# Optimization experiments

Hardware: AMD Instinct MI355X
Metric: run time of the kernel (lower is better)

Reference implementation:

```python
import jax, jax.numpy as jnp
import numpy as np


def setup_inputs() -> dict:
    key = jax.random.key(0)
    ks = jax.random.split(key, 7)
    B, S, D, H = 8, 1024, 1024, 16
    dk = D // H
    return {
        "q": jax.random.normal(ks[0], (B, S, D), dtype=jnp.float32),
        "k": jax.random.normal(ks[1], (B, S, D), dtype=jnp.float32),
        "v": jax.random.normal(ks[2], (B, S, D), dtype=jnp.float32),
        "Wq": jax.random.normal(ks[3], (H, dk, D), dtype=jnp.float32) * 0.03,
        "Wk": jax.random.normal(ks[4], (H, dk, D), dtype=jnp.float32) * 0.03,
        "Wv": jax.random.normal(ks[5], (dk, D), dtype=jnp.float32) * 0.03,
        "Wo": jax.random.normal(ks[6], (D, dk), dtype=jnp.float32) * 0.03,
    }


def reference(q, k, v, Wq, Wk, Wv, Wo):
    # per-head projections (Linear weight layout [out, in]); shared V projection
    dk = Wq.shape[1]
    qs = jnp.einsum("bsd,hed->bhse", q, Wq)          # [B,H,S,dk]
    ks_ = jnp.einsum("btd,hed->bhte", k, Wk)         # [B,H,S,dk]
    vs = jnp.einsum("btd,ed->bte", v, Wv)            # [B,S,dk] shared across heads
    scale = jnp.sqrt(jnp.asarray(dk, dtype=qs.dtype))
    scores = jnp.einsum("bhse,bhte->bhst", qs, ks_) / scale
    attn = jax.nn.softmax(scores, axis=-1)           # [B,H,Sq,Sk]
    heads = jnp.einsum("bhst,bte->bhse", attn, vs)   # [B,H,S,dk]
    head_mean = jnp.mean(heads, axis=1)              # mean over heads -> [B,S,dk]
    outputs = jnp.einsum("bse,de->bsd", head_mean, Wo)
    attn_out = jnp.transpose(attn, (0, 2, 1, 3))     # stacked at dim=2: [B,Sq,H,Sk]
    return outputs, attn_out
```

## Files before the change

### kernel.cpp

```cpp
#include <hip/hip_runtime.h>
#include <hip/hip_bf16.h>


typedef __attribute__((ext_vector_type(4))) float f32x4;
typedef __attribute__((ext_vector_type(8))) short bf16x8;
typedef __attribute__((ext_vector_type(4))) short short4v;
typedef __attribute__((ext_vector_type(2))) unsigned int uint2v;

#define MFMA16(a, b, c) __builtin_amdgcn_mfma_f32_16x16x32_bf16((a), (b), (c), 0, 0, 0)

__device__ __forceinline__ unsigned int rne16(float f) {
  unsigned int u = __float_as_uint(f);
  return u + 0x7fffu + ((u >> 16) & 1u);
}
__device__ __forceinline__ unsigned int pack2bf(float a, float b) {
  return (rne16(a) >> 16) | (rne16(b) & 0xffff0000u);
}
__device__ __forceinline__ short f2bf(float f) {
  return (short)(rne16(f) >> 16);
}
__device__ __forceinline__ float bf2f(short s) {
  return __uint_as_float(((unsigned int)(unsigned short)s) << 16);
}

__global__ __launch_bounds__(256) void proj_qk_kernel(
    const float* __restrict__ qin, const float* __restrict__ kin,
    const float* __restrict__ Wq, const float* __restrict__ Wk,
    __hip_bfloat16* __restrict__ qs, __hip_bfloat16* __restrict__ ks)
{
  const int K = 1024, N = 1024;
  __shared__ short a_lds[128][40];
  __shared__ short b_lds[128][40];
  const int tid  = threadIdx.x;
  const int lane = tid & 63, wid = tid >> 6;
  const int g = lane >> 4, r = lane & 15;
  const bool isK = blockIdx.y >= 8;
  const float* A = isK ? kin : qin;
  const float* W = isK ? Wk : Wq;
  __hip_bfloat16* C = isK ? ks : qs;
  const float scale = isK ? 1.0f : 0.125f;
  const int m0 = blockIdx.x * 128;
  const int n0 = (blockIdx.y & 7) * 128;
  const int wm = (wid >> 1) * 64, wn = (wid & 1) * 64;
  const int lrow = tid >> 3, lcol = (tid & 7) * 4;

  f32x4 acc[4][4];
#pragma unroll
  for (int i = 0; i < 4; ++i)
#pragma unroll
    for (int j = 0; j < 4; ++j) acc[i][j] = (f32x4){0.f, 0.f, 0.f, 0.f};

  for (int k0 = 0; k0 < K; k0 += 32) {
    float4 av[4], wv[4];
#pragma unroll
    for (int p = 0; p < 4; ++p) {
      av[p] = *(const float4*)&A[(m0 + lrow + p * 32) * K + k0 + lcol];
      wv[p] = *(const float4*)&W[(n0 + lrow + p * 32) * K + k0 + lcol];
    }
    __syncthreads();
#pragma unroll
    for (int p = 0; p < 4; ++p) {
      uint2v ua = {pack2bf(av[p].x, av[p].y), pack2bf(av[p].z, av[p].w)};
      uint2v uw = {pack2bf(wv[p].x, wv[p].y), pack2bf(wv[p].z, wv[p].w)};
      *(uint2v*)&a_lds[lrow + p * 32][lcol] = ua;
      *(uint2v*)&b_lds[lrow + p * 32][lcol] = uw;
    }
    __syncthreads();
    bf16x8 af[4], bf[4];
#pragma unroll
    for (int t = 0; t < 4; ++t) {
      af[t] = *(bf16x8*)&a_lds[wm + t * 16 + r][g * 8];
      bf[t] = *(bf16x8*)&b_lds[wn + t * 16 + r][g * 8];
    }
#pragma unroll
    for (int mt = 0; mt < 4; ++mt)
#pragma unroll
      for (int nt = 0; nt < 4; ++nt)
        acc[mt][nt] = MFMA16(af[mt], bf[nt], acc[mt][nt]);
  }

#pragma unroll
  for (int mt = 0; mt < 4; ++mt)
#pragma unroll
    for (int nt = 0; nt < 4; ++nt) {
      const int n = n0 + wn + nt * 16 + r;
#pragma unroll
      for (int j = 0; j < 4; ++j) {
        const int m = m0 + wm + mt * 16 + 4 * g + j;
        C[m * N + n] = __float2bfloat16(acc[mt][nt][j] * scale);
      }
    }
}

__global__ __launch_bounds__(256) void proj_v_kernel(
    const float* __restrict__ vin, const float* __restrict__ Wv,
    __hip_bfloat16* __restrict__ vsT)
{
  const int K = 1024;
  __shared__ short a_lds[128][40];
  __shared__ short b_lds[64][40];
  const int tid  = threadIdx.x;
  const int lane = tid & 63, wid = tid >> 6;
  const int g = lane >> 4, r = lane & 15;
  const int m0 = blockIdx.x * 128;
  const int wm = wid * 32;
  const int lrow = tid >> 3, lcol = (tid & 7) * 4;

  f32x4 acc[2][4];
#pragma unroll
  for (int i = 0; i < 2; ++i)
#pragma unroll
    for (int j = 0; j < 4; ++j) acc[i][j] = (f32x4){0.f, 0.f, 0.f, 0.f};

  for (int k0 = 0; k0 < K; k0 += 32) {
    float4 av[4], wv2[2];
#pragma unroll
    for (int p = 0; p < 4; ++p)
      av[p] = *(const float4*)&vin[(m0 + lrow + p * 32) * K + k0 + lcol];
#pragma unroll
    for (int p = 0; p < 2; ++p)
      wv2[p] = *(const float4*)&Wv[(lrow + p * 32) * K + k0 + lcol];
    __syncthreads();
#pragma unroll
    for (int p = 0; p < 4; ++p) {
      uint2v ua = {pack2bf(av[p].x, av[p].y), pack2bf(av[p].z, av[p].w)};
      *(uint2v*)&a_lds[lrow + p * 32][lcol] = ua;
    }
#pragma unroll
    for (int p = 0; p < 2; ++p) {
      uint2v uw = {pack2bf(wv2[p].x, wv2[p].y), pack2bf(wv2[p].z, wv2[p].w)};
      *(uint2v*)&b_lds[lrow + p * 32][lcol] = uw;
    }
    __syncthreads();
    bf16x8 af[2], bf[4];
#pragma unroll
    for (int t = 0; t < 2; ++t) af[t] = *(bf16x8*)&a_lds[wm + t * 16 + r][g * 8];
#pragma unroll
    for (int t = 0; t < 4; ++t) bf[t] = *(bf16x8*)&b_lds[t * 16 + r][g * 8];
#pragma unroll
    for (int mt = 0; mt < 2; ++mt)
#pragma unroll
      for (int nt = 0; nt < 4; ++nt)
        acc[mt][nt] = MFMA16(af[mt], bf[nt], acc[mt][nt]);
  }

#pragma unroll
  for (int mt = 0; mt < 2; ++mt)
#pragma unroll
    for (int nt = 0; nt < 4; ++nt) {
      const int e = nt * 16 + r;
#pragma unroll
      for (int j = 0; j < 4; ++j) {
        const int m = m0 + wm + mt * 16 + 4 * g + j;
        const int b = m >> 10, t = m & 1023;
        vsT[b * 65536 + e * 1024 + t] = __float2bfloat16(acc[mt][nt][j]);
      }
    }
}

__global__ __launch_bounds__(256, 4) void attn_kernel(
    const __hip_bfloat16* __restrict__ qs_, const __hip_bfloat16* __restrict__ ks_,
    const __hip_bfloat16* __restrict__ vsT_, float* __restrict__ attn_out,
    __hip_bfloat16* __restrict__ heads_)
{
  const int S = 1024, H = 16;
  const int tid = threadIdx.x, lane = tid & 63, kc = tid >> 6;
  const int g = lane >> 4, r = lane & 15;
  const int h = blockIdx.y, b = blockIdx.z;
  const int bh = b * H + h;
  const int qrow = blockIdx.x * 16;

  __shared__ short p_big[4][16][260];
  __shared__ float l_lds[4][16];
  __shared__ float inv_lds[16];
  float (*heads_ov)[16][80] = (float (*)[16][80])p_big;

  const short* qsp = (const short*)qs_;
  const short* ksp = (const short*)ks_;
  const short* vsp = (const short*)vsT_;
  short* headsp = (short*)heads_;

  const int qidx = (b * S + qrow + r) * 1024 + h * 64;
  const bf16x8 qf0 = *(const bf16x8*)&qsp[qidx + g * 8];
  const bf16x8 qf1 = *(const bf16x8*)&qsp[qidx + 32 + g * 8];
  const int kbase = (b * S + kc * 256 + r) * 1024 + h * 64 + g * 8;

  unsigned int pk[32];
  float lsa0 = 0.f, lsa1 = 0.f, lsa2 = 0.f, lsa3 = 0.f;
#pragma unroll
  for (int i = 0; i < 4; ++i) {
    const int t0 = i * 64;
    bf16x8 kf[8];
#pragma unroll
    for (int u = 0; u < 4; ++u) {
      kf[2 * u]     = *(const bf16x8*)&ksp[kbase + (t0 + 16 * u) * 1024];
      kf[2 * u + 1] = *(const bf16x8*)&ksp[kbase + (t0 + 16 * u) * 1024 + 32];
    }
    float es[4];
#pragma unroll
    for (int u = 0; u < 4; ++u) {
      f32x4 s = (f32x4){0.f, 0.f, 0.f, 0.f};
      s = MFMA16(kf[2 * u], qf0, s);
      s = MFMA16(kf[2 * u + 1], qf1, s);
      const float e0 = __expf(s[0]), e1 = __expf(s[1]);
      const float e2 = __expf(s[2]), e3 = __expf(s[3]);
      pk[i * 8 + 2 * u]     = pack2bf(e0, e1);
      pk[i * 8 + 2 * u + 1] = pack2bf(e2, e3);
      es[u] = (e0 + e1) + (e2 + e3);
    }
    lsa0 += es[0]; lsa1 += es[1]; lsa2 += es[2]; lsa3 += es[3];
  }
  float ls = (lsa0 + lsa1) + (lsa2 + lsa3);
  ls += __shfl_xor(ls, 16);
  ls += __shfl_xor(ls, 32);
  if (g == 0) l_lds[kc][r] = ls;
  __syncthreads();
  {
    const float lf = (l_lds[0][r] + l_lds[1][r]) + (l_lds[2][r] + l_lds[3][r]);
    if (kc == 0 && g == 0) inv_lds[r] = 1.f / lf;
  }

#pragma unroll
  for (int j = 0; j < 8; ++j) {
    uint2v w0 = {pk[4 * j + 0], pk[4 * j + 1]};
    uint2v w1 = {pk[4 * j + 2], pk[4 * j + 3]};
    *(uint2v*)&p_big[kc][r][j * 32 + 4 * g] = w0;
    *(uint2v*)&p_big[kc][r][j * 32 + 16 + 4 * g] = w1;
  }
  __syncthreads();

  f32x4 hacc[4];
#pragma unroll
  for (int i = 0; i < 4; ++i) hacc[i] = (f32x4){0.f, 0.f, 0.f, 0.f};
  const int vbase = b * 65536 + r * 1024 + g * 8 + kc * 256;

#pragma unroll
  for (int j = 0; j < 8; ++j) {
    const int tcl = j * 32;
    bf16x8 vf[4];
#pragma unroll
    for (int nt = 0; nt < 4; ++nt)
      vf[nt] = *(const bf16x8*)&vsp[vbase + nt * 16384 + tcl];
    const bf16x8 pa = *(bf16x8*)&p_big[kc][r][tcl + g * 8];
#pragma unroll
    for (int nt = 0; nt < 4; ++nt)
      hacc[nt] = MFMA16(pa, vf[nt], hacc[nt]);
  }

  {
    const int half = lane >> 5, l32 = lane & 31;
#pragma unroll
    for (int rp = 0; rp < 8; ++rp) {
      const int row = rp * 2 + half;
      const bf16x8 pe = *(const bf16x8*)&p_big[kc][row][l32 * 8];
      const float invr = inv_lds[row];
      f32x4 o0, o1;
      o0[0] = bf2f(pe[0]) * invr; o0[1] = bf2f(pe[1]) * invr;
      o0[2] = bf2f(pe[2]) * invr; o0[3] = bf2f(pe[3]) * invr;
      o1[0] = bf2f(pe[4]) * invr; o1[1] = bf2f(pe[5]) * invr;
      o1[2] = bf2f(pe[6]) * invr; o1[3] = bf2f(pe[7]) * invr;
      const int base = ((b * S + qrow + row) * H + h) * S + kc * 256 + l32 * 8;
      __builtin_nontemporal_store(o0, (f32x4*)&attn_out[base]);
      __builtin_nontemporal_store(o1, (f32x4*)&attn_out[base + 4]);
    }
  }
  __syncthreads();

#pragma unroll
  for (int nt = 0; nt < 4; ++nt)
#pragma unroll
    for (int j = 0; j < 4; ++j)
      heads_ov[kc][4 * g + j][nt * 16 + r] = hacc[nt][j];
  __syncthreads();

  {
    const int row = tid >> 4, c4 = (tid & 15) * 4;
    const float invr = inv_lds[row];
    short4v hv;
#pragma unroll
    for (int i = 0; i < 4; ++i) {
      const float s4 = (heads_ov[0][row][c4 + i] + heads_ov[1][row][c4 + i]) +
                       (heads_ov[2][row][c4 + i] + heads_ov[3][row][c4 + i]);
      hv[i] = f2bf(s4 * invr);
    }
    *(short4v*)&headsp[(bh * S + qrow + row) * 64 + c4] = hv;
  }
}

__global__ __launch_bounds__(256) void out_kernel(
    const __hip_bfloat16* __restrict__ heads_, const float* __restrict__ Wo,
    float* __restrict__ out)
{
  __shared__ float hm[16][64];
  const int tid = threadIdx.x;
  const int m0 = blockIdx.x * 16;
  const short* headsp = (const short*)heads_;

  {
    const int row = tid >> 4, e4 = (tid & 15) * 4;
    const int m = m0 + row, b = m >> 10, s = m & 1023;
    float a0 = 0.f, a1 = 0.f, a2 = 0.f, a3 = 0.f;
    for (int hh = 0; hh < 16; ++hh) {
      const short4v hv =
          *(const short4v*)&headsp[((b * 16 + hh) * 1024 + s) * 64 + e4];
      a0 += bf2f(hv[0]); a1 += bf2f(hv[1]); a2 += bf2f(hv[2]); a3 += bf2f(hv[3]);
    }
    const float sc = 1.f / 16.f;
    hm[row][e4 + 0] = a0 * sc; hm[row][e4 + 1] = a1 * sc;
    hm[row][e4 + 2] = a2 * sc; hm[row][e4 + 3] = a3 * sc;
  }
  __syncthreads();

  for (int c = 0; c < 4; ++c) {
    const int d = c * 256 + tid;
    float4 wo4[16];
#pragma unroll
    for (int i = 0; i < 16; ++i) wo4[i] = *(const float4*)&Wo[d * 64 + i * 4];
    for (int row = 0; row < 16; ++row) {
      float a = 0.f;
#pragma unroll
      for (int i = 0; i < 16; ++i) {
        const float4 h4 = *(const float4*)&hm[row][i * 4];
        a += h4.x * wo4[i].x + h4.y * wo4[i].y + h4.z * wo4[i].z + h4.w * wo4[i].w;
      }
      out[(m0 + row) * 1024 + d] = a;
    }
  }
}

extern "C" void kernel_launch(void* const* d_in, const int* in_sizes, int n_in,
                              void* d_out, int out_size, void* d_ws, size_t ws_size,
                              hipStream_t stream) {
  const float* q  = (const float*)d_in[0];
  const float* k  = (const float*)d_in[1];
  const float* v  = (const float*)d_in[2];
  const float* Wq = (const float*)d_in[3];
  const float* Wk = (const float*)d_in[4];
  const float* Wv = (const float*)d_in[5];
  const float* Wo = (const float*)d_in[6];

  float* out0 = (float*)d_out;
  float* attn = out0 + (size_t)8 * 1024 * 1024;

  char* ws = (char*)d_ws;
  __hip_bfloat16* qs    = (__hip_bfloat16*)(ws);
  __hip_bfloat16* ksbuf = (__hip_bfloat16*)(ws + (16u << 20));
  __hip_bfloat16* vsT   = (__hip_bfloat16*)(ws + (32u << 20));
  __hip_bfloat16* heads = (__hip_bfloat16*)(ws + (33u << 20));

  proj_qk_kernel<<<dim3(64, 16), dim3(256), 0, stream>>>(q, k, Wq, Wk, qs, ksbuf);
  proj_v_kernel<<<dim3(64), dim3(256), 0, stream>>>(v, Wv, vsT);
  attn_kernel<<<dim3(64, 16, 8), dim3(256), 0, stream>>>(qs, ksbuf, vsT, attn, heads);
  out_kernel<<<dim3(512), dim3(256), 0, stream>>>(heads, Wo, out0);
}
```

Baseline: 424.8 us.

## Replace LDS cross-wave head reduction with fp32 global atomics and drop barriers

Each wave now adds its partial P·V result for its key chunk directly into an fp32 heads buffer with atomicAdd, after scaling by the row normaliser obtained via shuffles. This removes the LDS staging, two barriers and the bf16 repack at the end of the attention kernel, and one barrier is replaced by a wave-local waitcnt. The cost is a new zeroing kernel over a 32 MB fp32 buffer, 16 atomics per lane, and twice the heads traffic read by out_kernel. Correctness of the waitcnt relies on each wave reading only its own p_big slice.

After: 445.7 us. +4.9%, slower.

```diff
diff --git a/kernel.cpp b/kernel.cpp
--- a/kernel.cpp
+++ b/kernel.cpp
@@ -4,7 +4,6 @@
 
 typedef __attribute__((ext_vector_type(4))) float f32x4;
 typedef __attribute__((ext_vector_type(8))) short bf16x8;
-typedef __attribute__((ext_vector_type(4))) short short4v;
 typedef __attribute__((ext_vector_type(2))) unsigned int uint2v;
 
 #define MFMA16(a, b, c) __builtin_amdgcn_mfma_f32_16x16x32_bf16((a), (b), (c), 0, 0, 0)
@@ -16,11 +15,14 @@
 __device__ __forceinline__ unsigned int pack2bf(float a, float b) {
   return (rne16(a) >> 16) | (rne16(b) & 0xffff0000u);
 }
-__device__ __forceinline__ short f2bf(float f) {
-  return (short)(rne16(f) >> 16);
-}
 __device__ __forceinline__ float bf2f(short s) {
   return __uint_as_float(((unsigned int)(unsigned short)s) << 16);
+}
+
+__global__ __launch_bounds__(256) void zero_heads_kernel(float* __restrict__ p) {
+  const int i = blockIdx.x * 256 + threadIdx.x;
+  f32x4 z = (f32x4){0.f, 0.f, 0.f, 0.f};
+  *(f32x4*)&p[i * 4] = z;
 }
 
 __global__ __launch_bounds__(256) void proj_qk_kernel(
@@ -161,7 +163,7 @@
 __global__ __launch_bounds__(256, 4) void attn_kernel(
     const __hip_bfloat16* __restrict__ qs_, const __hip_bfloat16* __restrict__ ks_,
     const __hip_bfloat16* __restrict__ vsT_, float* __restrict__ attn_out,
-    __hip_bfloat16* __restrict__ heads_)
+    float* __restrict__ heads_f32)
 {
   const int S = 1024, H = 16;
   const int tid = threadIdx.x, lane = tid & 63, kc = tid >> 6;
@@ -172,13 +174,10 @@
 
   __shared__ short p_big[4][16][260];
   __shared__ float l_lds[4][16];
-  __shared__ float inv_lds[16];
-  float (*heads_ov)[16][80] = (float (*)[16][80])p_big;
 
   const short* qsp = (const short*)qs_;
   const short* ksp = (const short*)ks_;
   const short* vsp = (const short*)vsT_;
-  short* headsp = (short*)heads_;
 
   const int qidx = (b * S + qrow + r) * 1024 + h * 64;
   const bf16x8 qf0 = *(const bf16x8*)&qsp[qidx + g * 8];
@@ -215,10 +214,11 @@
   ls += __shfl_xor(ls, 32);
   if (g == 0) l_lds[kc][r] = ls;
   __syncthreads();
-  {
-    const float lf = (l_lds[0][r] + l_lds[1][r]) + (l_lds[2][r] + l_lds[3][r]);
-    if (kc == 0 && g == 0) inv_lds[r] = 1.f / lf;
-  }
+  const float lf = (l_lds[0][r] + l_lds[1][r]) + (l_lds[2][r] + l_lds[3][r]);
+  const float inv = 1.f / lf;
+  float invq[4];
+#pragma unroll
+  for (int j = 0; j < 4; ++j) invq[j] = __shfl(inv, 4 * g + j);
 
 #pragma unroll
   for (int j = 0; j < 8; ++j) {
@@ -227,7 +227,7 @@
     *(uint2v*)&p_big[kc][r][j * 32 + 4 * g] = w0;
     *(uint2v*)&p_big[kc][r][j * 32 + 16 + 4 * g] = w1;
   }
-  __syncthreads();
+  asm volatile("s_waitcnt lgkmcnt(0)" ::: "memory");
 
   f32x4 hacc[4];
 #pragma unroll
@@ -248,12 +248,22 @@
   }
 
   {
+    const int hbase = (bh * S + qrow) * 64;
+#pragma unroll
+    for (int nt = 0; nt < 4; ++nt)
+#pragma unroll
+      for (int j = 0; j < 4; ++j)
+        atomicAdd(&heads_f32[hbase + (4 * g + j) * 64 + nt * 16 + r],
+                  hacc[nt][j] * invq[j]);
+  }
+
+  {
     const int half = lane >> 5, l32 = lane & 31;
 #pragma unroll
     for (int rp = 0; rp < 8; ++rp) {
       const int row = rp * 2 + half;
+      const float invr = __shfl(inv, row);
       const bf16x8 pe = *(const bf16x8*)&p_big[kc][row][l32 * 8];
-      const float invr = inv_lds[row];
       f32x4 o0, o1;
       o0[0] = bf2f(pe[0]) * invr; o0[1] = bf2f(pe[1]) * invr;
       o0[2] = bf2f(pe[2]) * invr; o0[3] = bf2f(pe[3]) * invr;
@@ -264,50 +274,28 @@
       __builtin_nontemporal_store(o1, (f32x4*)&attn_out[base + 4]);
     }
   }
-  __syncthreads();
-
-#pragma unroll
-  for (int nt = 0; nt < 4; ++nt)
-#pragma unroll
-    for (int j = 0; j < 4; ++j)
-      heads_ov[kc][4 * g + j][nt * 16 + r] = hacc[nt][j];
-  __syncthreads();
-
-  {
-    const int row = tid >> 4, c4 = (tid & 15) * 4;
-    const float invr = inv_lds[row];
-    short4v hv;
-#pragma unroll
-    for (int i = 0; i < 4; ++i) {
-      const float s4 = (heads_ov[0][row][c4 + i] + heads_ov[1][row][c4 + i]) +
-                       (heads_ov[2][row][c4 + i] + heads_ov[3][row][c4 + i]);
-      hv[i] = f2bf(s4 * invr);
-    }
-    *(short4v*)&headsp[(bh * S + qrow + row) * 64 + c4] = hv;
-  }
 }
 
 __global__ __launch_bounds__(256) void out_kernel(
-    const __hip_bfloat16* __restrict__ heads_, const float* __restrict__ Wo,
+    const float* __restrict__ heads_f32, const float* __restrict__ Wo,
     float* __restrict__ out)
 {
   __shared__ float hm[16][64];
   const int tid = threadIdx.x;
   const int m0 = blockIdx.x * 16;
-  const short* headsp = (const short*)heads_;
 
   {
     const int row = tid >> 4, e4 = (tid & 15) * 4;
     const int m = m0 + row, b = m >> 10, s = m & 1023;
-    float a0 = 0.f, a1 = 0.f, a2 = 0.f, a3 = 0.f;
+    float4 a = make_float4(0.f, 0.f, 0.f, 0.f);
     for (int hh = 0; hh < 16; ++hh) {
-      const short4v hv =
-          *(const short4v*)&headsp[((b * 16 + hh) * 1024 + s) * 64 + e4];
-      a0 += bf2f(hv[0]); a1 += bf2f(hv[1]); a2 += bf2f(hv[2]); a3 += bf2f(hv[3]);
+      const float4 hv =
+          *(const float4*)&heads_f32[((b * 16 + hh) * 1024 + s) * 64 + e4];
+      a.x += hv.x; a.y += hv.y; a.z += hv.z; a.w += hv.w;
     }
     const float sc = 1.f / 16.f;
-    hm[row][e4 + 0] = a0 * sc; hm[row][e4 + 1] = a1 * sc;
-    hm[row][e4 + 2] = a2 * sc; hm[row][e4 + 3] = a3 * sc;
+    hm[row][e4 + 0] = a.x * sc; hm[row][e4 + 1] = a.y * sc;
+    hm[row][e4 + 2] = a.z * sc; hm[row][e4 + 3] = a.w * sc;
   }
   __syncthreads();
 
@@ -346,8 +334,9 @@
   __hip_bfloat16* qs    = (__hip_bfloat16*)(ws);
   __hip_bfloat16* ksbuf = (__hip_bfloat16*)(ws + (16u << 20));
   __hip_bfloat16* vsT   = (__hip_bfloat16*)(ws + (32u << 20));
-  __hip_bfloat16* heads = (__hip_bfloat16*)(ws + (33u << 20));
-
+  float*          heads = (float*)(ws + (34u << 20));
+
+  zero_heads_kernel<<<dim3(8192), dim3(256), 0, stream>>>(heads);
   proj_qk_kernel<<<dim3(64, 16), dim3(256), 0, stream>>>(q, k, Wq, Wk, qs, ksbuf);
   proj_v_kernel<<<dim3(64), dim3(256), 0, stream>>>(v, Wv, vsT);
   attn_kernel<<<dim3(64, 16, 8), dim3(256), 0, stream>>>(qs, ksbuf, vsT, attn, heads);
```
